# Optimization experiments

Hardware: AMD Instinct MI355X
Metric: run time of the kernel (lower is better)

The kernel has to match this reference:

```python
import jax, jax.numpy as jnp
import numpy as np

B, S, D, H, K = 64, 512, 256, 4, 1  # batch, seq, dim, heads, seeds; key_dim == D (Keras quirk)
EPS = 1e-6


def setup_inputs() -> dict:
    key = jax.random.key(0)
    ks = jax.random.split(key, 12)
    s = 1.0 / np.sqrt(D)
    return {
        "x": jax.random.normal(ks[0], (B, S, D), jnp.float32),
        "mask": jax.random.randint(ks[1], (B, S), 0, 2, jnp.int32),
        "seeds": jax.random.normal(ks[2], (K, D), jnp.float32) * s,
        "Wq": jax.random.normal(ks[3], (D, H, D), jnp.float32) * s,
        "bq": jnp.zeros((H, D), jnp.float32),
        "Wk": jax.random.normal(ks[4], (D, H, D), jnp.float32) * s,
        "bk": jnp.zeros((H, D), jnp.float32),
        "Wv": jax.random.normal(ks[5], (D, H, D), jnp.float32) * s,
        "bv": jnp.zeros((H, D), jnp.float32),
        "Wo": jax.random.normal(ks[6], (H, D, D), jnp.float32) * s,
        "bo": jnp.zeros((D,), jnp.float32),
        "gamma": jnp.ones((D,), jnp.float32),
        "beta": jnp.zeros((D,), jnp.float32),
    }


def reference(x, mask, seeds, Wq, bq, Wk, bk, Wv, bv, Wo, bo, gamma, beta):
    # Projections (Keras MHA: per-head dim = key_dim = D)
    q = jnp.einsum("kd,dhe->khe", seeds, Wq) + bq           # [K,H,D] (shared across batch)
    kp = jnp.einsum("bsd,dhe->bshe", x, Wk) + bk            # [B,S,H,D]
    vp = jnp.einsum("bsd,dhe->bshe", x, Wv) + bv            # [B,S,H,D]
    scores = jnp.einsum("khe,bshe->bhks", q, kp) / jnp.sqrt(jnp.float32(D))  # [B,H,K,S]
    adder = (1.0 - mask.astype(scores.dtype))[:, None, None, :] * -1e9
    attn = jax.nn.softmax(scores + adder, axis=-1)
    o = jnp.einsum("bhks,bshe->bkhe", attn, vp)             # [B,K,H,D]
    h = jnp.einsum("bkhe,hed->bkd", o, Wo) + bo             # attention output
    h = seeds[None] + h                                     # residual (dropout off: inference)
    mu = jnp.mean(h, axis=-1, keepdims=True)
    var = jnp.mean(jnp.square(h - mu), axis=-1, keepdims=True)
    h = (h - mu) / jnp.sqrt(var + EPS) * gamma + beta
    return h[:, 0, :]                                       # [B,D]
```

## Files before the change

kernel.cpp:

```cpp
#include <hip/hip_runtime.h>
#include <hip/hip_bf16.h>
#include <math.h>

#define BB 64
#define SS 512
#define DD 256
#define HH 4
#define SCALE 0.0625f

__device__ inline float wave_red_sum(float v) {
#pragma unroll
    for (int off = 32; off > 0; off >>= 1) v += __shfl_xor(v, off, 64);
    return v;
}
__device__ inline float wave_red_max(float v) {
#pragma unroll
    for (int off = 32; off > 0; off >>= 1) v = fmaxf(v, __shfl_xor(v, off, 64));
    return v;
}

__global__ __launch_bounds__(256) void qp_kernel(const float* __restrict__ seeds,
                                                 const float* __restrict__ Wq,
                                                 float* __restrict__ qp) {
    int c = blockIdx.x, tid = threadIdx.x;
    __shared__ float sl[16];
    if (tid < 16) sl[tid] = seeds[c * 16 + tid];
    __syncthreads();
#pragma unroll
    for (int rep = 0; rep < 4; ++rep) {
        int i = tid + rep * 256;
        float acc = 0.f;
#pragma unroll
        for (int dl = 0; dl < 16; ++dl)
            acc += sl[dl] * Wq[(size_t)(c * 16 + dl) * (HH * DD) + i];
        qp[c * (HH * DD) + i] = acc;
    }
}

__global__ __launch_bounds__(256) void kq_kernel(const float* __restrict__ Wk,
                                                 const float* __restrict__ bk,
                                                 const float* __restrict__ bq,
                                                 const float* __restrict__ qp,
                                                 float* __restrict__ kqp,
                                                 float* __restrict__ kbp) {
    int h = blockIdx.x >> 2, es = blockIdx.x & 3;
    int d = threadIdx.x;
    __shared__ float ql[64];
    __shared__ float bkq[64];
    int e0 = es * 64;
    if (d < 64) {
        int i = h * DD + e0 + d;
        float qv = bq[i];
#pragma unroll
        for (int c = 0; c < 16; ++c) qv += qp[c * (HH * DD) + i];
        ql[d] = qv;
        bkq[d] = bk[i] * qv;
    }
    __syncthreads();
    const float4* w4 = reinterpret_cast<const float4*>(Wk + (size_t)d * (HH * DD) + h * DD + e0);
    const float4* q4 = reinterpret_cast<const float4*>(ql);
    float acc = 0.f;
#pragma unroll
    for (int e4 = 0; e4 < 16; ++e4) {
        float4 w = w4[e4], qq = q4[e4];
        acc += w.x * qq.x + w.y * qq.y + w.z * qq.z + w.w * qq.w;
    }
    kqp[(es * HH + h) * DD + d] = acc;
    if (d < 64) {
        float v = wave_red_sum(bkq[d]);
        if (d == 0) kbp[es * HH + h] = v;
    }
}

__global__ __launch_bounds__(256) void scores_kernel(const float* __restrict__ x,
                                                     const int* __restrict__ mask,
                                                     const float* __restrict__ kqp,
                                                     const float* __restrict__ kbp,
                                                     float* __restrict__ scores) {
    int b = blockIdx.x >> 2, st = blockIdx.x & 3;
    int tid = threadIdx.x;
    __shared__ float kql[HH][DD];
    __shared__ float kbl[HH];
    __shared__ float part[2][HH][128];
    for (int i = tid; i < HH * DD; i += 256) {
        int h = i >> 8, d = i & 255;
        float v = 0.f;
#pragma unroll
        for (int es = 0; es < 4; ++es) v += kqp[(es * HH + h) * DD + d];
        kql[h][d] = v;
    }
    if (tid < HH) {
        float v = 0.f;
#pragma unroll
        for (int es = 0; es < 4; ++es) v += kbp[es * HH + tid];
        kbl[tid] = v;
    }
    __syncthreads();

    int sl = tid & 127, half = tid >> 7;
    int s = st * 128 + sl;
    const float4* xr = reinterpret_cast<const float4*>(x + ((size_t)b * SS + s) * DD + half * 128);
    const float4* k0 = reinterpret_cast<const float4*>(&kql[0][half * 128]);
    const float4* k1 = reinterpret_cast<const float4*>(&kql[1][half * 128]);
    const float4* k2 = reinterpret_cast<const float4*>(&kql[2][half * 128]);
    const float4* k3 = reinterpret_cast<const float4*>(&kql[3][half * 128]);
    float a0 = 0.f, a1 = 0.f, a2 = 0.f, a3 = 0.f;
#pragma unroll 8
    for (int d4 = 0; d4 < 32; ++d4) {
        float4 xv = xr[d4];
        float4 w0 = k0[d4], w1 = k1[d4], w2 = k2[d4], w3 = k3[d4];
        a0 += xv.x * w0.x + xv.y * w0.y + xv.z * w0.z + xv.w * w0.w;
        a1 += xv.x * w1.x + xv.y * w1.y + xv.z * w1.z + xv.w * w1.w;
        a2 += xv.x * w2.x + xv.y * w2.y + xv.z * w2.z + xv.w * w2.w;
        a3 += xv.x * w3.x + xv.y * w3.y + xv.z * w3.z + xv.w * w3.w;
    }
    part[half][0][sl] = a0;
    part[half][1][sl] = a1;
    part[half][2][sl] = a2;
    part[half][3][sl] = a3;
    __syncthreads();
    if (half == 0) {
        float madd = (1.0f - (float)mask[b * SS + s]) * -1e9f;
#pragma unroll
        for (int h = 0; h < HH; ++h) {
            float v = part[0][h][sl] + part[1][h][sl] + kbl[h];
            scores[((size_t)(b * HH + h)) * SS + s] = v * SCALE + madd;
        }
    }
}

__global__ __launch_bounds__(256) void xbar_kernel(const float* __restrict__ x,
                                                   const float* __restrict__ scores,
                                                   float* __restrict__ xbarp) {
    int b = blockIdx.x >> 2, st = blockIdx.x & 3;
    int tid = threadIdx.x, wave = tid >> 6, lane = tid & 63;
    __shared__ float at[HH][SS];
    {
        float vals[8];
        float m = -1e30f;
        const float* sr = scores + ((size_t)(b * HH + wave)) * SS;
#pragma unroll
        for (int k = 0; k < 8; ++k) {
            vals[k] = sr[lane + 64 * k];
            m = fmaxf(m, vals[k]);
        }
        m = wave_red_max(m);
        float l = 0.f;
#pragma unroll
        for (int k = 0; k < 8; ++k) {
            vals[k] = __expf(vals[k] - m);
            l += vals[k];
        }
        l = wave_red_sum(l);
        float inv = 1.0f / l;
#pragma unroll
        for (int k = 0; k < 8; ++k) at[wave][lane + 64 * k] = vals[k] * inv;
    }
    __syncthreads();

    float a0 = 0.f, a1 = 0.f, a2 = 0.f, a3 = 0.f;
    const float* xb = x + ((size_t)b * SS + st * 128) * DD + tid;
#pragma unroll 4
    for (int s = 0; s < 128; ++s) {
        float xv = xb[(size_t)s * DD];
        int sg = st * 128 + s;
        a0 += at[0][sg] * xv;
        a1 += at[1][sg] * xv;
        a2 += at[2][sg] * xv;
        a3 += at[3][sg] * xv;
    }
    float* xo = xbarp + ((size_t)(b * 4 + st)) * (HH * DD);
    xo[0 * DD + tid] = a0;
    xo[1 * DD + tid] = a1;
    xo[2 * DD + tid] = a2;
    xo[3 * DD + tid] = a3;
}

__global__ __launch_bounds__(256) void ovwo_kernel(const float* __restrict__ xbarp,
                                                   const float* __restrict__ Wv,
                                                   const float* __restrict__ bv,
                                                   const float* __restrict__ Wo,
                                                   float* __restrict__ wop) {
    int b = blockIdx.x >> 2, h = blockIdx.x & 3;
    int tid = threadIdx.x;
    __shared__ float xl[DD];
    __shared__ float ol[DD];
    float v = 0.f;
#pragma unroll
    for (int st = 0; st < 4; ++st) v += xbarp[((size_t)(b * 4 + st)) * (HH * DD) + h * DD + tid];
    xl[tid] = v;
    __syncthreads();
    float acc = bv[h * DD + tid];
    const float* wv = Wv + h * DD + tid;
#pragma unroll 8
    for (int d = 0; d < DD; ++d) acc += xl[d] * wv[(size_t)d * (HH * DD)];
    ol[tid] = acc;
    __syncthreads();
    float acc2 = 0.f;
    const float* wo = Wo + (size_t)(h * DD) * DD + tid;
#pragma unroll 8
    for (int e = 0; e < DD; ++e) acc2 += ol[e] * wo[(size_t)e * DD];
    wop[((size_t)(b * HH + h)) * DD + tid] = acc2;
}

__global__ __launch_bounds__(256) void ln_kernel(const float* __restrict__ wop,
                                                 const float* __restrict__ bo,
                                                 const float* __restrict__ seeds,
                                                 const float* __restrict__ gamma,
                                                 const float* __restrict__ beta,
                                                 float* __restrict__ out) {
    __shared__ float r1[4], r2[4];
    int b = blockIdx.x, tid = threadIdx.x;
    int wave = tid >> 6, lane = tid & 63;
    float acc = bo[tid] + seeds[tid];
#pragma unroll
    for (int h = 0; h < HH; ++h) acc += wop[((size_t)(b * HH + h)) * DD + tid];

    float t = wave_red_sum(acc);
    if (lane == 0) r1[wave] = t;
    __syncthreads();
    float mu = (r1[0] + r1[1] + r1[2] + r1[3]) * (1.0f / DD);
    float dv = acc - mu;
    float t2 = wave_red_sum(dv * dv);
    if (lane == 0) r2[wave] = t2;
    __syncthreads();
    float var = (r2[0] + r2[1] + r2[2] + r2[3]) * (1.0f / DD);
    out[(size_t)b * DD + tid] = dv * rsqrtf(var + 1e-6f) * gamma[tid] + beta[tid];
}

extern "C" void kernel_launch(void* const* d_in, const int* in_sizes, int n_in,
                              void* d_out, int out_size, void* d_ws, size_t ws_size,
                              hipStream_t stream) {
    const float* x = (const float*)d_in[0];
    const int* mask = (const int*)d_in[1];
    const float* seeds = (const float*)d_in[2];
    const float* Wq = (const float*)d_in[3];
    const float* bq = (const float*)d_in[4];
    const float* Wk = (const float*)d_in[5];
    const float* bk = (const float*)d_in[6];
    const float* Wv = (const float*)d_in[7];
    const float* bv = (const float*)d_in[8];
    const float* Wo = (const float*)d_in[9];
    const float* bo = (const float*)d_in[10];
    const float* gamma = (const float*)d_in[11];
    const float* beta = (const float*)d_in[12];
    float* out = (float*)d_out;

    float* ws = (float*)d_ws;
    float* qp = ws;
    float* kqp = qp + 16384;
    float* kbp = kqp + 4096;
    float* scores = kbp + 16;
    float* xbarp = scores + 131072;
    float* wop = xbarp + 262144;

    qp_kernel<<<16, 256, 0, stream>>>(seeds, Wq, qp);
    kq_kernel<<<16, 256, 0, stream>>>(Wk, bk, bq, qp, kqp, kbp);
    scores_kernel<<<BB * 4, 256, 0, stream>>>(x, mask, kqp, kbp, scores);
    xbar_kernel<<<BB * 4, 256, 0, stream>>>(x, scores, xbarp);
    ovwo_kernel<<<BB * HH, 256, 0, stream>>>(xbarp, Wv, bv, Wo, wop);
    ln_kernel<<<BB, 256, 0, stream>>>(wop, bo, seeds, gamma, beta, out);
}
```

Baseline: 151.0 us.

## Fuse scores, softmax and weighted-x into one flash-style kernel reading x once

Result: faster. 140.7 us (-6.8%).

```diff
diff --git a/kernel.cpp b/kernel.cpp
--- a/kernel.cpp
+++ b/kernel.cpp
@@ -7,6 +7,7 @@
 #define DD 256
 #define HH 4
 #define SCALE 0.0625f
+#define PAD 261
 
 __device__ inline float wave_red_sum(float v) {
 #pragma unroll
@@ -37,146 +38,128 @@
     }
 }
 
-__global__ __launch_bounds__(256) void kq_kernel(const float* __restrict__ Wk,
-                                                 const float* __restrict__ bk,
-                                                 const float* __restrict__ bq,
-                                                 const float* __restrict__ qp,
-                                                 float* __restrict__ kqp,
-                                                 float* __restrict__ kbp) {
-    int h = blockIdx.x >> 2, es = blockIdx.x & 3;
-    int d = threadIdx.x;
-    __shared__ float ql[64];
-    __shared__ float bkq[64];
-    int e0 = es * 64;
-    if (d < 64) {
-        int i = h * DD + e0 + d;
-        float qv = bq[i];
-#pragma unroll
-        for (int c = 0; c < 16; ++c) qv += qp[c * (HH * DD) + i];
-        ql[d] = qv;
-        bkq[d] = bk[i] * qv;
-    }
-    __syncthreads();
-    const float4* w4 = reinterpret_cast<const float4*>(Wk + (size_t)d * (HH * DD) + h * DD + e0);
-    const float4* q4 = reinterpret_cast<const float4*>(ql);
+__global__ __launch_bounds__(256) void kqf_kernel(const float* __restrict__ Wk,
+                                                  const float* __restrict__ bk,
+                                                  const float* __restrict__ bq,
+                                                  const float* __restrict__ qp,
+                                                  float* __restrict__ kqf,
+                                                  float* __restrict__ kbg) {
+    int h = blockIdx.x >> 2, ds = blockIdx.x & 3;
+    int tid = threadIdx.x, w = tid >> 6, lane = tid & 63;
+    __shared__ float ql[DD];
+    __shared__ float red[4][64];
+    __shared__ float rb[4];
+    float qv = bq[h * DD + tid];
+#pragma unroll
+    for (int c = 0; c < 16; ++c) qv += qp[c * (HH * DD) + h * DD + tid];
+    ql[tid] = qv;
+    float bkv = bk[h * DD + tid] * qv;
+    float t1 = wave_red_sum(bkv);
+    if (lane == 0) rb[w] = t1;
+    __syncthreads();
+    if (tid == 0) kbg[h] = rb[0] + rb[1] + rb[2] + rb[3];
+    int dl = tid & 63, ec = tid >> 6;
+    int d = ds * 64 + dl;
+    const float4* wrow = reinterpret_cast<const float4*>(Wk + (size_t)d * (HH * DD) + h * DD + ec * 64);
+    const float4* qq4 = reinterpret_cast<const float4*>(&ql[ec * 64]);
     float acc = 0.f;
 #pragma unroll
     for (int e4 = 0; e4 < 16; ++e4) {
-        float4 w = w4[e4], qq = q4[e4];
-        acc += w.x * qq.x + w.y * qq.y + w.z * qq.z + w.w * qq.w;
-    }
-    kqp[(es * HH + h) * DD + d] = acc;
-    if (d < 64) {
-        float v = wave_red_sum(bkq[d]);
-        if (d == 0) kbp[es * HH + h] = v;
-    }
-}
-
-__global__ __launch_bounds__(256) void scores_kernel(const float* __restrict__ x,
-                                                     const int* __restrict__ mask,
-                                                     const float* __restrict__ kqp,
-                                                     const float* __restrict__ kbp,
-                                                     float* __restrict__ scores) {
-    int b = blockIdx.x >> 2, st = blockIdx.x & 3;
-    int tid = threadIdx.x;
-    __shared__ float kql[HH][DD];
-    __shared__ float kbl[HH];
-    __shared__ float part[2][HH][128];
-    for (int i = tid; i < HH * DD; i += 256) {
-        int h = i >> 8, d = i & 255;
-        float v = 0.f;
-#pragma unroll
-        for (int es = 0; es < 4; ++es) v += kqp[(es * HH + h) * DD + d];
-        kql[h][d] = v;
-    }
-    if (tid < HH) {
-        float v = 0.f;
-#pragma unroll
-        for (int es = 0; es < 4; ++es) v += kbp[es * HH + tid];
-        kbl[tid] = v;
-    }
-    __syncthreads();
-
-    int sl = tid & 127, half = tid >> 7;
-    int s = st * 128 + sl;
-    const float4* xr = reinterpret_cast<const float4*>(x + ((size_t)b * SS + s) * DD + half * 128);
-    const float4* k0 = reinterpret_cast<const float4*>(&kql[0][half * 128]);
-    const float4* k1 = reinterpret_cast<const float4*>(&kql[1][half * 128]);
-    const float4* k2 = reinterpret_cast<const float4*>(&kql[2][half * 128]);
-    const float4* k3 = reinterpret_cast<const float4*>(&kql[3][half * 128]);
-    float a0 = 0.f, a1 = 0.f, a2 = 0.f, a3 = 0.f;
-#pragma unroll 8
-    for (int d4 = 0; d4 < 32; ++d4) {
-        float4 xv = xr[d4];
-        float4 w0 = k0[d4], w1 = k1[d4], w2 = k2[d4], w3 = k3[d4];
-        a0 += xv.x * w0.x + xv.y * w0.y + xv.z * w0.z + xv.w * w0.w;
-        a1 += xv.x * w1.x + xv.y * w1.y + xv.z * w1.z + xv.w * w1.w;
-        a2 += xv.x * w2.x + xv.y * w2.y + xv.z * w2.z + xv.w * w2.w;
-        a3 += xv.x * w3.x + xv.y * w3.y + xv.z * w3.z + xv.w * w3.w;
-    }
-    part[half][0][sl] = a0;
-    part[half][1][sl] = a1;
-    part[half][2][sl] = a2;
-    part[half][3][sl] = a3;
-    __syncthreads();
-    if (half == 0) {
-        float madd = (1.0f - (float)mask[b * SS + s]) * -1e9f;
-#pragma unroll
-        for (int h = 0; h < HH; ++h) {
-            float v = part[0][h][sl] + part[1][h][sl] + kbl[h];
-            scores[((size_t)(b * HH + h)) * SS + s] = v * SCALE + madd;
+        float4 wv = wrow[e4], qq = qq4[e4];
+        acc += wv.x * qq.x + wv.y * qq.y + wv.z * qq.z + wv.w * qq.w;
+    }
+    red[ec][dl] = acc;
+    __syncthreads();
+    if (tid < 64) kqf[h * DD + ds * 64 + tid] = red[0][tid] + red[1][tid] + red[2][tid] + red[3][tid];
+}
+
+__global__ __launch_bounds__(256) void flash_kernel(const float* __restrict__ x,
+                                                    const int* __restrict__ mask,
+                                                    const float* __restrict__ kqg,
+                                                    const float* __restrict__ kbg,
+                                                    float* __restrict__ xp,
+                                                    float* __restrict__ mt,
+                                                    float* __restrict__ lt) {
+    int b = blockIdx.x >> 3, st = blockIdx.x & 7;
+    int tid = threadIdx.x, w = tid >> 6, lane = tid & 63;
+    __shared__ float xt[64][PAD];
+    __shared__ __align__(16) float part[4][2][64];
+    float* sc = &part[0][0][0];
+
+    const float4* xg = reinterpret_cast<const float4*>(x + ((size_t)b * SS + st * 64) * DD);
+#pragma unroll
+    for (int c = 0; c < 16; ++c) {
+        int f = c * 256 + tid;
+        float4 v = xg[f];
+        int row = f >> 6, col = (f & 63) * 4;
+        xt[row][col + 0] = v.x;
+        xt[row][col + 1] = v.y;
+        xt[row][col + 2] = v.z;
+        xt[row][col + 3] = v.w;
+    }
+    __syncthreads();
+
+    int s = lane;
+    int hp = w >> 1, kk = w & 1;
+    int off = __builtin_amdgcn_readfirstlane(hp * 2 * DD + kk * 128);
+    const float* kA = kqg + off;
+    const float* kB = kqg + off + DD;
+    const float* xrow = &xt[s][kk * 128];
+    float a0 = 0.f, a1 = 0.f;
+#pragma unroll 16
+    for (int k = 0; k < 128; ++k) {
+        float xv = xrow[k];
+        a0 = fmaf(xv, kA[k], a0);
+        a1 = fmaf(xv, kB[k], a1);
+    }
+    part[w][0][s] = a0;
+    part[w][1][s] = a1;
+    __syncthreads();
+
+    int h = w;
+    float v = part[2 * (h >> 1)][h & 1][s] + part[2 * (h >> 1) + 1][h & 1][s];
+    float score = (v + kbg[h]) * SCALE + (1.f - (float)mask[b * SS + st * 64 + s]) * -1e9f;
+    float m = wave_red_max(score);
+    float p = __expf(score - m);
+    float l = wave_red_sum(p);
+    __syncthreads();
+    sc[h * 64 + s] = p;
+    if (lane == 0) {
+        mt[blockIdx.x * 4 + h] = m;
+        lt[blockIdx.x * 4 + h] = l;
+    }
+    __syncthreads();
+
+    float o0 = 0.f, o1 = 0.f, o2 = 0.f, o3 = 0.f;
+#pragma unroll 4
+    for (int sb = 0; sb < 16; ++sb) {
+        float4 p0 = *reinterpret_cast<const float4*>(&sc[0 * 64 + 4 * sb]);
+        float4 p1 = *reinterpret_cast<const float4*>(&sc[1 * 64 + 4 * sb]);
+        float4 p2 = *reinterpret_cast<const float4*>(&sc[2 * 64 + 4 * sb]);
+        float4 p3 = *reinterpret_cast<const float4*>(&sc[3 * 64 + 4 * sb]);
+#pragma unroll
+        for (int j = 0; j < 4; ++j) {
+            float xv = xt[4 * sb + j][tid];
+            float pj0 = (j == 0) ? p0.x : (j == 1) ? p0.y : (j == 2) ? p0.z : p0.w;
+            float pj1 = (j == 0) ? p1.x : (j == 1) ? p1.y : (j == 2) ? p1.z : p1.w;
+            float pj2 = (j == 0) ? p2.x : (j == 1) ? p2.y : (j == 2) ? p2.z : p2.w;
+            float pj3 = (j == 0) ? p3.x : (j == 1) ? p3.y : (j == 2) ? p3.z : p3.w;
+            o0 = fmaf(pj0, xv, o0);
+            o1 = fmaf(pj1, xv, o1);
+            o2 = fmaf(pj2, xv, o2);
+            o3 = fmaf(pj3, xv, o3);
         }
     }
-}
-
-__global__ __launch_bounds__(256) void xbar_kernel(const float* __restrict__ x,
-                                                   const float* __restrict__ scores,
-                                                   float* __restrict__ xbarp) {
-    int b = blockIdx.x >> 2, st = blockIdx.x & 3;
-    int tid = threadIdx.x, wave = tid >> 6, lane = tid & 63;
-    __shared__ float at[HH][SS];
-    {
-        float vals[8];
-        float m = -1e30f;
-        const float* sr = scores + ((size_t)(b * HH + wave)) * SS;
-#pragma unroll
-        for (int k = 0; k < 8; ++k) {
-            vals[k] = sr[lane + 64 * k];
-            m = fmaxf(m, vals[k]);
-        }
-        m = wave_red_max(m);
-        float l = 0.f;
-#pragma unroll
-        for (int k = 0; k < 8; ++k) {
-            vals[k] = __expf(vals[k] - m);
-            l += vals[k];
-        }
-        l = wave_red_sum(l);
-        float inv = 1.0f / l;
-#pragma unroll
-        for (int k = 0; k < 8; ++k) at[wave][lane + 64 * k] = vals[k] * inv;
-    }
-    __syncthreads();
-
-    float a0 = 0.f, a1 = 0.f, a2 = 0.f, a3 = 0.f;
-    const float* xb = x + ((size_t)b * SS + st * 128) * DD + tid;
-#pragma unroll 4
-    for (int s = 0; s < 128; ++s) {
-        float xv = xb[(size_t)s * DD];
-        int sg = st * 128 + s;
-        a0 += at[0][sg] * xv;
-        a1 += at[1][sg] * xv;
-        a2 += at[2][sg] * xv;
-        a3 += at[3][sg] * xv;
-    }
-    float* xo = xbarp + ((size_t)(b * 4 + st)) * (HH * DD);
-    xo[0 * DD + tid] = a0;
-    xo[1 * DD + tid] = a1;
-    xo[2 * DD + tid] = a2;
-    xo[3 * DD + tid] = a3;
-}
-
-__global__ __launch_bounds__(256) void ovwo_kernel(const float* __restrict__ xbarp,
+    float* xpo = xp + (size_t)blockIdx.x * 4 * DD;
+    xpo[0 * DD + tid] = o0;
+    xpo[1 * DD + tid] = o1;
+    xpo[2 * DD + tid] = o2;
+    xpo[3 * DD + tid] = o3;
+}
+
+__global__ __launch_bounds__(256) void ovwo_kernel(const float* __restrict__ xp,
+                                                   const float* __restrict__ mt,
+                                                   const float* __restrict__ lt,
                                                    const float* __restrict__ Wv,
                                                    const float* __restrict__ bv,
                                                    const float* __restrict__ Wo,
@@ -185,10 +168,21 @@
     int tid = threadIdx.x;
     __shared__ float xl[DD];
     __shared__ float ol[DD];
-    float v = 0.f;
-#pragma unroll
-    for (int st = 0; st < 4; ++st) v += xbarp[((size_t)(b * 4 + st)) * (HH * DD) + h * DD + tid];
-    xl[tid] = v;
+    float M = -3.0e38f;
+#pragma unroll
+    for (int t = 0; t < 8; ++t) M = fmaxf(M, mt[(b * 8 + t) * 4 + h]);
+    float L = 0.f;
+    float co[8];
+#pragma unroll
+    for (int t = 0; t < 8; ++t) {
+        co[t] = __expf(mt[(b * 8 + t) * 4 + h] - M);
+        L += lt[(b * 8 + t) * 4 + h] * co[t];
+    }
+    float invL = 1.0f / L;
+    float xb = 0.f;
+#pragma unroll
+    for (int t = 0; t < 8; ++t) xb += co[t] * xp[((size_t)(b * 8 + t) * 4 + h) * DD + tid];
+    xl[tid] = xb * invL;
     __syncthreads();
     float acc = bv[h * DD + tid];
     const float* wv = Wv + h * DD + tid;
@@ -196,11 +190,11 @@
     for (int d = 0; d < DD; ++d) acc += xl[d] * wv[(size_t)d * (HH * DD)];
     ol[tid] = acc;
     __syncthreads();
-    float acc2 = 0.f;
+    float a2 = 0.f;
     const float* wo = Wo + (size_t)(h * DD) * DD + tid;
 #pragma unroll 8
-    for (int e = 0; e < DD; ++e) acc2 += ol[e] * wo[(size_t)e * DD];
-    wop[((size_t)(b * HH + h)) * DD + tid] = acc2;
+    for (int e = 0; e < DD; ++e) a2 += ol[e] * wo[(size_t)e * DD];
+    wop[((size_t)(b * HH + h)) * DD + tid] = a2;
 }
 
 __global__ __launch_bounds__(256) void ln_kernel(const float* __restrict__ wop,
@@ -211,18 +205,18 @@
                                                  float* __restrict__ out) {
     __shared__ float r1[4], r2[4];
     int b = blockIdx.x, tid = threadIdx.x;
-    int wave = tid >> 6, lane = tid & 63;
+    int w = tid >> 6, lane = tid & 63;
     float acc = bo[tid] + seeds[tid];
 #pragma unroll
     for (int h = 0; h < HH; ++h) acc += wop[((size_t)(b * HH + h)) * DD + tid];
 
     float t = wave_red_sum(acc);
-    if (lane == 0) r1[wave] = t;
+    if (lane == 0) r1[w] = t;
     __syncthreads();
     float mu = (r1[0] + r1[1] + r1[2] + r1[3]) * (1.0f / DD);
     float dv = acc - mu;
     float t2 = wave_red_sum(dv * dv);
-    if (lane == 0) r2[wave] = t2;
+    if (lane == 0) r2[w] = t2;
     __syncthreads();
     float var = (r2[0] + r2[1] + r2[2] + r2[3]) * (1.0f / DD);
     out[(size_t)b * DD + tid] = dv * rsqrtf(var + 1e-6f) * gamma[tid] + beta[tid];
@@ -247,17 +241,17 @@
     float* out = (float*)d_out;
 
     float* ws = (float*)d_ws;
-    float* qp = ws;
-    float* kqp = qp + 16384;
-    float* kbp = kqp + 4096;
-    float* scores = kbp + 16;
-    float* xbarp = scores + 131072;
-    float* wop = xbarp + 262144;
+    float* qp  = ws;
+    float* kqf = ws + 16384;
+    float* kbg = ws + 17408;
+    float* mt  = ws + 17424;
+    float* lt  = ws + 19472;
+    float* xp  = ws + 21520;
+    float* wop = ws + 545808;
 
     qp_kernel<<<16, 256, 0, stream>>>(seeds, Wq, qp);
-    kq_kernel<<<16, 256, 0, stream>>>(Wk, bk, bq, qp, kqp, kbp);
-    scores_kernel<<<BB * 4, 256, 0, stream>>>(x, mask, kqp, kbp, scores);
-    xbar_kernel<<<BB * 4, 256, 0, stream>>>(x, scores, xbarp);
-    ovwo_kernel<<<BB * HH, 256, 0, stream>>>(xbarp, Wv, bv, Wo, wop);
+    kqf_kernel<<<16, 256, 0, stream>>>(Wk, bk, bq, qp, kqf, kbg);
+    flash_kernel<<<BB * 8, 256, 0, stream>>>(x, mask, kqf, kbg, xp, mt, lt);
+    ovwo_kernel<<<BB * HH, 256, 0, stream>>>(xp, mt, lt, Wv, bv, Wo, wop);
     ln_kernel<<<BB, 256, 0, stream>>>(wop, bo, seeds, gamma, beta, out);
 }
```
